# Kernel optimization log

Measured on AMD Instinct MI355X. Metric: run time of the kernel, lower is better.

Reference implementation:

```python
import jax, jax.numpy as jnp
import numpy as np
import math

B, S, D, H = 4, 1024, 1024, 16
DK = D // H


def setup_inputs() -> dict:
    key = jax.random.key(0)
    ks = jax.random.split(key, 14)
    inp = {
        "query": jax.random.normal(ks[0], (B, S, D), dtype=jnp.float32),
        "key": jax.random.normal(ks[1], (B, S, D), dtype=jnp.float32),
        "value": jax.random.normal(ks[2], (B, S, D), dtype=jnp.float32),
        "attention_bias": jax.random.normal(ks[3], (B, S, S, H), dtype=jnp.float32),
        "mask": jax.random.randint(ks[4], (B, S), 0, 2).astype(bool),
    }
    scale = 0.02
    inp["Wq"] = jax.random.normal(ks[5], (D, D), dtype=jnp.float32) * scale
    inp["bq"] = jnp.zeros((D,), dtype=jnp.float32)
    inp["Wk"] = jax.random.normal(ks[6], (D, D), dtype=jnp.float32) * scale
    inp["bk"] = jnp.zeros((D,), dtype=jnp.float32)
    inp["Wv"] = jax.random.normal(ks[7], (D, D), dtype=jnp.float32) * scale
    inp["bv"] = jnp.zeros((D,), dtype=jnp.float32)
    inp["Wo"] = jax.random.normal(ks[8], (D, D), dtype=jnp.float32) * scale
    inp["bo"] = jnp.zeros((D,), dtype=jnp.float32)
    return inp


def reference(query, key, value, attention_bias, mask, Wq, bq, Wk, bk, Wv, bv, Wo, bo):
    # projections (torch Linear: x @ W.T + b), split heads -> [B,H,S,DK]
    def proj(x, W, b):
        y = x @ W.T + b
        return y.reshape(B, S, H, DK).transpose(0, 2, 1, 3)

    q = proj(query, Wq, bq)
    k = proj(key, Wk, bk)
    v = proj(value, Wv, bv)

    bias = attention_bias.transpose(0, 3, 1, 2)  # [B,H,S,S]
    scores = (jnp.einsum("bhqd,bhkd->bhqk", q, k) + bias) / math.sqrt(DK)

    # pairwise mask: outer product of per-token mask, broadcast over heads
    pm = (mask[:, None, :, None] & mask[:, None, None, :])  # [B,1,S,S]
    scores = jnp.where(pm, scores, jnp.float32(-1e9))

    p_attn = jax.nn.softmax(scores, axis=-1)  # dropout is identity in eval
    x = jnp.einsum("bhqk,bhkd->bhqd", p_attn, v)
    x = x.transpose(0, 2, 1, 3).reshape(B, S, D)
    return x @ Wo.T + bo
```

## Files before the change

kernel.cpp:

```cpp
#include <hip/hip_runtime.h>
#include <hip/hip_bf16.h>
#include <math.h>

#define B_ 4
#define S_ 1024
#define D_ 1024
#define H_ 16
#define DK_ 64

typedef short bf16x8 __attribute__((ext_vector_type(8)));
typedef float f32x4 __attribute__((ext_vector_type(4)));

#define MFMA(a, b, c) __builtin_amdgcn_mfma_f32_16x16x32_bf16(a, b, c, 0, 0, 0)

#define GLDS(gp, lp)                                                        \
    __builtin_amdgcn_global_load_lds(                                       \
        (const __attribute__((address_space(1))) void*)(const void*)(gp),   \
        (__attribute__((address_space(3))) void*)(void*)(lp), 16, 0, 0)

static __device__ __forceinline__ unsigned short f2bf(float f) {
    __hip_bfloat16 h = __float2bfloat16(f);
    return *reinterpret_cast<unsigned short*>(&h);
}
static __device__ __forceinline__ float bf2f(unsigned short u) {
    unsigned int x = ((unsigned int)u) << 16;
    union { unsigned int i; float f; } c; c.i = x; return c.f;
}

__global__ __launch_bounds__(256) void cvt3(
    const float* __restrict__ a, const float* __restrict__ b, const float* __restrict__ c,
    unsigned short* __restrict__ oa, unsigned short* __restrict__ ob, unsigned short* __restrict__ oc)
{
    int bx = blockIdx.x;
    int which = bx >> 12;
    const float* in = which == 0 ? a : which == 1 ? b : c;
    unsigned short* out = which == 0 ? oa : which == 1 ? ob : oc;
    int i = (bx & 4095) * 256 + threadIdx.x;
    float4 v = ((const float4*)in)[i];
    ushort4 o;
    o.x = f2bf(v.x); o.y = f2bf(v.y); o.z = f2bf(v.z); o.w = f2bf(v.w);
    ((ushort4*)out)[i] = o;
}

__global__ __launch_bounds__(256) void cvt4(
    const float* __restrict__ a, const float* __restrict__ b,
    const float* __restrict__ c, const float* __restrict__ d,
    unsigned short* __restrict__ oa, unsigned short* __restrict__ ob,
    unsigned short* __restrict__ oc, unsigned short* __restrict__ od)
{
    int bx = blockIdx.x;
    int which = bx >> 10;
    const float* in = which == 0 ? a : which == 1 ? b : which == 2 ? c : d;
    unsigned short* out = which == 0 ? oa : which == 1 ? ob : which == 2 ? oc : od;
    int i = (bx & 1023) * 256 + threadIdx.x;
    float4 v = ((const float4*)in)[i];
    ushort4 o;
    o.x = f2bf(v.x); o.y = f2bf(v.y); o.z = f2bf(v.z); o.w = f2bf(v.w);
    ((ushort4*)out)[i] = o;
}

__global__ __launch_bounds__(256) void prep_bias(
    const float* __restrict__ bias, const int* __restrict__ mask,
    unsigned short* __restrict__ biasP)
{
    const int t = threadIdx.x;
    const int h = t & 15, u = t >> 4;
    const int x = blockIdx.x;
    const int kt = x & 15, q16 = (x >> 4) & 63, b = x >> 10;

    const unsigned short NEG = f2bf(-28672.f);

    int mk[4];
    #pragma unroll
    for (int j = 0; j < 4; ++j) mk[j] = mask[b * 1024 + kt * 64 + j * 16 + u];

    const float* bb = bias + (((size_t)(b * 1024 + q16 * 16) * 1024) + kt * 64) * 16 + h;
    unsigned short* ob = biasP + ((((size_t)(b * 16 + h) * 64 + q16) * 16 + kt) * 64) * 16;

    #pragma unroll
    for (int quad = 0; quad < 4; ++quad) {
        bf16x8 v0, v1;
        #pragma unroll
        for (int r = 0; r < 4; ++r) {
            int q = quad * 4 + r;
            int mq = mask[b * 1024 + q16 * 16 + q];
            #pragma unroll
            for (int j = 0; j < 4; ++j) {
                float v = bb[((size_t)q * 1024 + j * 16 + u) * 16];
                unsigned short pv = (mq && mk[j]) ? f2bf(v * 0.125f) : NEG;
                if (j < 2) v0[j * 4 + r] = (short)pv;
                else       v1[(j - 2) * 4 + r] = (short)pv;
            }
        }
        unsigned short* dst = ob + (size_t)(quad * 16 + u) * 16;
        *(bf16x8*)(dst) = v0;
        *(bf16x8*)(dst + 8) = v1;
    }
}

__global__ __launch_bounds__(256, 2) void gemm128(
    const unsigned short* __restrict__ X0, const unsigned short* __restrict__ X1,
    const unsigned short* __restrict__ X2,
    const unsigned short* __restrict__ W0, const unsigned short* __restrict__ W1,
    const unsigned short* __restrict__ W2,
    const float* __restrict__ bv0, const float* __restrict__ bv1,
    const float* __restrict__ bv2,
    void* __restrict__ Y0, void* __restrict__ Y1, void* __restrict__ Y2,
    const int* __restrict__ mask, int mode_ovr)
{
    __shared__ unsigned short As[128 * 32];
    __shared__ unsigned short Bs[128 * 32];

    const int z = blockIdx.z;
    const unsigned short* X = z == 0 ? X0 : z == 1 ? X1 : X2;
    const unsigned short* W = z == 0 ? W0 : z == 1 ? W1 : W2;
    const float* bvec = z == 0 ? bv0 : z == 1 ? bv1 : bv2;
    void* Yv = z == 0 ? Y0 : z == 1 ? Y1 : Y2;
    const int mode = mode_ovr >= 0 ? mode_ovr : z;

    const int t = threadIdx.x;
    const int w = t >> 6, l = t & 63;
    const int lane16 = l & 15, quad = l >> 4;
    const int m0 = blockIdx.y * 128, n0 = blockIdx.x * 128;
    const int wr = w >> 1, wc = w & 1;

    const int srow = w * 16 + (l >> 2);
    const unsigned short* agp = X + (size_t)(m0 + srow) * 1024 + (l & 3) * 8;
    const unsigned short* bgp = W + (size_t)(n0 + srow) * 1024 + (l & 3) * 8;
    unsigned short* alp = As + w * 512 + l * 8;
    unsigned short* blp = Bs + w * 512 + l * 8;

    f32x4 zero = {0.f, 0.f, 0.f, 0.f};
    f32x4 acc[4][4];
    #pragma unroll
    for (int i = 0; i < 4; ++i)
        #pragma unroll
        for (int j = 0; j < 4; ++j) acc[i][j] = zero;

    for (int kt = 0; kt < 1024; kt += 32) {
        GLDS(agp + kt, alp);
        GLDS(agp + kt + 64 * 1024, alp + 2048);
        GLDS(bgp + kt, blp);
        GLDS(bgp + kt + 64 * 1024, blp + 2048);
        __syncthreads();

        bf16x8 af[4], bfv[4];
        #pragma unroll
        for (int i = 0; i < 4; ++i)
            af[i] = *(const bf16x8*)(As + (wr * 64 + i * 16 + lane16) * 32 + quad * 8);
        #pragma unroll
        for (int j = 0; j < 4; ++j)
            bfv[j] = *(const bf16x8*)(Bs + (wc * 64 + j * 16 + lane16) * 32 + quad * 8);

        #pragma unroll
        for (int i = 0; i < 4; ++i)
            #pragma unroll
            for (int j = 0; j < 4; ++j)
                acc[i][j] = MFMA(af[i], bfv[j], acc[i][j]);
        __syncthreads();
    }

    float bvl[4];
    #pragma unroll
    for (int j = 0; j < 4; ++j) bvl[j] = bvec[n0 + wc * 64 + j * 16 + lane16];

    if (mode == 2) {
        const int bb = m0 >> 10;
        const int sb = (m0 & 1023) + wr * 64;
        #pragma unroll
        for (int i = 0; i < 4; ++i) {
            #pragma unroll
            for (int j = 0; j < 4; ++j) {
                int n = n0 + wc * 64 + j * 16 + lane16;
                ushort4 pk;
                pk.x = f2bf(acc[i][j][0] + bvl[j]);
                pk.y = f2bf(acc[i][j][1] + bvl[j]);
                pk.z = f2bf(acc[i][j][2] + bvl[j]);
                pk.w = f2bf(acc[i][j][3] + bvl[j]);
                int s = sb + i * 16 + quad * 4;
                *(ushort4*)((unsigned short*)Yv + ((size_t)(bb * 1024 + n)) * 1024 + s) = pk;
            }
        }
    } else if (mode == 3) {
        float* Y = (float*)Yv;
        #pragma unroll
        for (int i = 0; i < 4; ++i)
            #pragma unroll
            for (int j = 0; j < 4; ++j) {
                int n = n0 + wc * 64 + j * 16 + lane16;
                #pragma unroll
                for (int r = 0; r < 4; ++r) {
                    size_t m = m0 + wr * 64 + i * 16 + quad * 4 + r;
                    Y[m * 1024 + n] = acc[i][j][r] + bvl[j];
                }
            }
    } else {
        unsigned short* Y = (unsigned short*)Yv;
        #pragma unroll
        for (int i = 0; i < 4; ++i) {
            int mrow[4];
            #pragma unroll
            for (int r = 0; r < 4; ++r)
                mrow[r] = (mode == 0) ? mask[m0 + wr * 64 + i * 16 + quad * 4 + r] : 1;
            #pragma unroll
            for (int j = 0; j < 4; ++j) {
                int n = n0 + wc * 64 + j * 16 + lane16;
                #pragma unroll
                for (int r = 0; r < 4; ++r) {
                    size_t m = m0 + wr * 64 + i * 16 + quad * 4 + r;
                    float val = acc[i][j][r] + bvl[j];
                    if (mode == 0) val = mrow[r] ? val * 0.125f : 0.f;
                    Y[m * 1024 + n] = f2bf(val);
                }
            }
        }
    }
}

__global__ __launch_bounds__(256, 2) void attn_mfma(
    const unsigned short* __restrict__ Qp, const unsigned short* __restrict__ Kp,
    const unsigned short* __restrict__ VpT, const unsigned short* __restrict__ biasP,
    unsigned short* __restrict__ Xp)
{
    __shared__ unsigned short Ks[64 * 64];
    __shared__ unsigned short Vs[64 * 64];
    __shared__ unsigned short Ps[4][16 * 72];

    const int t = threadIdx.x;
    const int w = t >> 6, l = t & 63;
    const int lane16 = l & 15, quad = l >> 4;

    const int bid = blockIdx.x;
    const int bh = bid & 63, qt = bid >> 6;
    const int h = bh & 15, b = bh >> 4;
    const int q0 = qt * 64;
    const int qrow0 = q0 + w * 16;
    const int q16 = qt * 4 + w;

    bf16x8 qf[2];
    #pragma unroll
    for (int c = 0; c < 2; ++c)
        qf[c] = *(const bf16x8*)(Qp + (size_t)(b * 1024 + qrow0 + lane16) * 1024
                                 + h * 64 + c * 32 + quad * 8);

    const unsigned short* bp = biasP
        + ((((size_t)(b * 16 + h) * 64 + q16) * 16) * 64 + l) * 16;

    const int krow = w * 8 + (l >> 3);
    const int kgran = (l & 7) ^ ((l >> 3) & 7);
    const unsigned short* kg = Kp + (size_t)(b * 1024 + krow) * 1024 + h * 64 + kgran * 8;
    unsigned short* klp = Ks + w * 512 + l * 8;
    const unsigned short* vg = VpT + ((size_t)(b * 16 + h) * 64 + krow) * 1024 + kgran * 8;
    unsigned short* vlp = Vs + w * 512 + l * 8;

    f32x4 zero = {0.f, 0.f, 0.f, 0.f};
    f32x4 o[4];
    #pragma unroll
    for (int j = 0; j < 4; ++j) o[j] = zero;
    float m_i[4] = {-1e30f, -1e30f, -1e30f, -1e30f};
    float l_i[4] = {0.f, 0.f, 0.f, 0.f};

    for (int kt16 = 0; kt16 < 16; ++kt16) {
        const int k0 = kt16 * 64;
        GLDS(kg + (size_t)k0 * 1024, klp);
        GLDS(kg + (size_t)(k0 + 32) * 1024, klp + 32 * 64);
        GLDS(vg + k0, vlp);
        GLDS(vg + k0 + 32 * 1024, vlp + 32 * 64);

        bf16x8 bfr0 = *(const bf16x8*)(bp + (size_t)kt16 * 1024);
        bf16x8 bfr1 = *(const bf16x8*)(bp + (size_t)kt16 * 1024 + 8);
        __syncthreads();

        f32x4 s[4];
        #pragma unroll
        for (int j = 0; j < 4; ++j) {
            s[j] = zero;
            #pragma unroll
            for (int c = 0; c < 2; ++c) {
                bf16x8 kf = *(const bf16x8*)(Ks + (j * 16 + lane16) * 64
                                             + (((c * 4 + quad) ^ (lane16 & 7)) * 8));
                s[j] = MFMA(qf[c], kf, s[j]);
            }
        }

        float sc[4][4];
        #pragma unroll
        for (int e = 0; e < 8; ++e) {
            sc[e >> 2][e & 3]       = s[e >> 2][e & 3]       + bf2f((unsigned short)bfr0[e]);
            sc[2 + (e >> 2)][e & 3] = s[2 + (e >> 2)][e & 3] + bf2f((unsigned short)bfr1[e]);
        }

        float p[4][4];
        #pragma unroll
        for (int r = 0; r < 4; ++r) {
            float mx = fmaxf(fmaxf(sc[0][r], sc[1][r]), fmaxf(sc[2][r], sc[3][r]));
            #pragma unroll
            for (int d = 1; d < 16; d <<= 1) mx = fmaxf(mx, __shfl_xor(mx, d, 64));
            float mnew = fmaxf(m_i[r], mx);
            float alpha = __expf(m_i[r] - mnew);
            m_i[r] = mnew;
            float sum = 0.f;
            #pragma unroll
            for (int j = 0; j < 4; ++j) {
                p[j][r] = __expf(sc[j][r] - mnew);
                sum += p[j][r];
            }
            #pragma unroll
            for (int d = 1; d < 16; d <<= 1) sum += __shfl_xor(sum, d, 64);
            l_i[r] = l_i[r] * alpha + sum;
            #pragma unroll
            for (int jd = 0; jd < 4; ++jd) o[jd][r] *= alpha;
        }

        #pragma unroll
        for (int j = 0; j < 4; ++j)
            #pragma unroll
            for (int r = 0; r < 4; ++r)
                Ps[w][(quad * 4 + r) * 72 + j * 16 + lane16] = f2bf(p[j][r]);
        asm volatile("" ::: "memory");

        bf16x8 pf[2];
        #pragma unroll
        for (int c = 0; c < 2; ++c)
            pf[c] = *(const bf16x8*)(&Ps[w][lane16 * 72 + c * 32 + quad * 8]);

        #pragma unroll
        for (int jd = 0; jd < 4; ++jd)
            #pragma unroll
            for (int c = 0; c < 2; ++c) {
                bf16x8 vf = *(const bf16x8*)(Vs + (jd * 16 + lane16) * 64
                                             + (((c * 4 + quad) ^ (lane16 & 7)) * 8));
                o[jd] = MFMA(pf[c], vf, o[jd]);
            }
        __syncthreads();
    }

    float inv[4];
    #pragma unroll
    for (int r = 0; r < 4; ++r) inv[r] = 1.0f / l_i[r];

    #pragma unroll
    for (int jd = 0; jd < 4; ++jd)
        #pragma unroll
        for (int r = 0; r < 4; ++r)
            Xp[(size_t)(b * 1024 + qrow0 + quad * 4 + r) * 1024
               + h * 64 + jd * 16 + lane16] = f2bf(o[jd][r] * inv[r]);
}

extern "C" void kernel_launch(void* const* d_in, const int* in_sizes, int n_in,
                              void* d_out, int out_size, void* d_ws, size_t ws_size,
                              hipStream_t stream)
{
    const float* query = (const float*)d_in[0];
    const float* key   = (const float*)d_in[1];
    const float* value = (const float*)d_in[2];
    const float* abias = (const float*)d_in[3];
    const int*   mask  = (const int*)d_in[4];
    const float* Wq = (const float*)d_in[5];
    const float* bq = (const float*)d_in[6];
    const float* Wk = (const float*)d_in[7];
    const float* bk = (const float*)d_in[8];
    const float* Wv = (const float*)d_in[9];
    const float* bv = (const float*)d_in[10];
    const float* Wo = (const float*)d_in[11];
    const float* bo = (const float*)d_in[12];
    float* out = (float*)d_out;

    const size_t T = (size_t)B_ * S_ * D_;
    const size_t WSZ = (size_t)D_ * D_;
    const size_t BPSZ = (size_t)B_ * H_ * S_ * S_;
    unsigned short* p = (unsigned short*)d_ws;
    unsigned short* biasP = p;  p += BPSZ;
    unsigned short* qb  = p;  p += T;
    unsigned short* kb  = p;  p += T;
    unsigned short* vb  = p;  p += T;
    unsigned short* wqb = p;  p += WSZ;
    unsigned short* wkb = p;  p += WSZ;
    unsigned short* wvb = p;  p += WSZ;
    unsigned short* wob = p;  p += WSZ;
    unsigned short* Qpj = p;  p += T;
    unsigned short* Kpj = p;  p += T;
    unsigned short* VpT = p;  p += T;
    unsigned short* Xpj = p;  p += T;

    cvt3<<<dim3(3 * 4096), 256, 0, stream>>>(query, key, value, qb, kb, vb);
    cvt4<<<dim3(4 * 1024), 256, 0, stream>>>(Wq, Wk, Wv, Wo, wqb, wkb, wvb, wob);
    prep_bias<<<dim3(4096), 256, 0, stream>>>(abias, mask, biasP);

    gemm128<<<dim3(8, 32, 3), 256, 0, stream>>>(
        qb, kb, vb, wqb, wkb, wvb, bq, bk, bv,
        (void*)Qpj, (void*)Kpj, (void*)VpT, mask, -1);

    attn_mfma<<<dim3(1024), 256, 0, stream>>>(Qpj, Kpj, VpT, biasP, Xpj);

    gemm128<<<dim3(8, 32, 1), 256, 0, stream>>>(
        Xpj, Xpj, Xpj, wob, wob, wob, bo, bo, bo,
        (void*)out, (void*)out, (void*)out, mask, 3);
}
```

Baseline: 583.5 us.

## Merge prep kernels, interleave bias prep with QKV GEMM, double-buffer attention K/V

Merges the two conversion kernels into one launch. Interleaves the memory-bound bias/mask preprocessing blocks with the compute-bound QKV projection blocks in a single grid so the two can overlap. The attention kernel now double-buffers K/V tiles in LDS, prefetches the next bias fragment, drops the trailing barrier and uses an XOR swizzle for the P scratch buffer. The output projection switches to 128x64 tiles to double the block count. This trades more LDS and register pressure, plus a heterogeneous block mix, for better overlap and occupancy.

```diff
diff --git a/kernel.cpp b/kernel.cpp
--- a/kernel.cpp
+++ b/kernel.cpp
@@ -27,192 +27,177 @@
     union { unsigned int i; float f; } c; c.i = x; return c.f;
 }
 
-__global__ __launch_bounds__(256) void cvt3(
+__global__ __launch_bounds__(256) void cvt_all(
     const float* __restrict__ a, const float* __restrict__ b, const float* __restrict__ c,
-    unsigned short* __restrict__ oa, unsigned short* __restrict__ ob, unsigned short* __restrict__ oc)
+    const float* __restrict__ wa, const float* __restrict__ wb,
+    const float* __restrict__ wc, const float* __restrict__ wd,
+    unsigned short* __restrict__ oa, unsigned short* __restrict__ ob, unsigned short* __restrict__ oc,
+    unsigned short* __restrict__ owa, unsigned short* __restrict__ owb,
+    unsigned short* __restrict__ owc, unsigned short* __restrict__ owd)
 {
     int bx = blockIdx.x;
-    int which = bx >> 12;
-    const float* in = which == 0 ? a : which == 1 ? b : c;
-    unsigned short* out = which == 0 ? oa : which == 1 ? ob : oc;
-    int i = (bx & 4095) * 256 + threadIdx.x;
+    const float* in; unsigned short* out; int i;
+    if (bx < 12288) {
+        int which = bx >> 12;
+        in  = which == 0 ? a : which == 1 ? b : c;
+        out = which == 0 ? oa : which == 1 ? ob : oc;
+        i = (bx & 4095) * 256 + threadIdx.x;
+    } else {
+        int b2 = bx - 12288;
+        int which = b2 >> 10;
+        in  = which == 0 ? wa : which == 1 ? wb : which == 2 ? wc : wd;
+        out = which == 0 ? owa : which == 1 ? owb : which == 2 ? owc : owd;
+        i = (b2 & 1023) * 256 + threadIdx.x;
+    }
     float4 v = ((const float4*)in)[i];
     ushort4 o;
     o.x = f2bf(v.x); o.y = f2bf(v.y); o.z = f2bf(v.z); o.w = f2bf(v.w);
     ((ushort4*)out)[i] = o;
 }
 
-__global__ __launch_bounds__(256) void cvt4(
-    const float* __restrict__ a, const float* __restrict__ b,
-    const float* __restrict__ c, const float* __restrict__ d,
-    unsigned short* __restrict__ oa, unsigned short* __restrict__ ob,
-    unsigned short* __restrict__ oc, unsigned short* __restrict__ od)
-{
-    int bx = blockIdx.x;
-    int which = bx >> 10;
-    const float* in = which == 0 ? a : which == 1 ? b : which == 2 ? c : d;
-    unsigned short* out = which == 0 ? oa : which == 1 ? ob : which == 2 ? oc : od;
-    int i = (bx & 1023) * 256 + threadIdx.x;
-    float4 v = ((const float4*)in)[i];
-    ushort4 o;
-    o.x = f2bf(v.x); o.y = f2bf(v.y); o.z = f2bf(v.z); o.w = f2bf(v.w);
-    ((ushort4*)out)[i] = o;
-}
-
-__global__ __launch_bounds__(256) void prep_bias(
-    const float* __restrict__ bias, const int* __restrict__ mask,
-    unsigned short* __restrict__ biasP)
-{
-    const int t = threadIdx.x;
-    const int h = t & 15, u = t >> 4;
-    const int x = blockIdx.x;
-    const int kt = x & 15, q16 = (x >> 4) & 63, b = x >> 10;
-
-    const unsigned short NEG = f2bf(-28672.f);
-
-    int mk[4];
-    #pragma unroll
-    for (int j = 0; j < 4; ++j) mk[j] = mask[b * 1024 + kt * 64 + j * 16 + u];
-
-    const float* bb = bias + (((size_t)(b * 1024 + q16 * 16) * 1024) + kt * 64) * 16 + h;
-    unsigned short* ob = biasP + ((((size_t)(b * 16 + h) * 64 + q16) * 16 + kt) * 64) * 16;
-
-    #pragma unroll
-    for (int quad = 0; quad < 4; ++quad) {
-        bf16x8 v0, v1;
-        #pragma unroll
-        for (int r = 0; r < 4; ++r) {
-            int q = quad * 4 + r;
-            int mq = mask[b * 1024 + q16 * 16 + q];
-            #pragma unroll
-            for (int j = 0; j < 4; ++j) {
-                float v = bb[((size_t)q * 1024 + j * 16 + u) * 16];
-                unsigned short pv = (mq && mk[j]) ? f2bf(v * 0.125f) : NEG;
-                if (j < 2) v0[j * 4 + r] = (short)pv;
-                else       v1[(j - 2) * 4 + r] = (short)pv;
-            }
-        }
-        unsigned short* dst = ob + (size_t)(quad * 16 + u) * 16;
-        *(bf16x8*)(dst) = v0;
-        *(bf16x8*)(dst + 8) = v1;
-    }
-}
-
-__global__ __launch_bounds__(256, 2) void gemm128(
+__global__ __launch_bounds__(256, 2) void qkv_prep(
     const unsigned short* __restrict__ X0, const unsigned short* __restrict__ X1,
     const unsigned short* __restrict__ X2,
     const unsigned short* __restrict__ W0, const unsigned short* __restrict__ W1,
     const unsigned short* __restrict__ W2,
     const float* __restrict__ bv0, const float* __restrict__ bv1,
     const float* __restrict__ bv2,
-    void* __restrict__ Y0, void* __restrict__ Y1, void* __restrict__ Y2,
-    const int* __restrict__ mask, int mode_ovr)
+    unsigned short* __restrict__ Y0, unsigned short* __restrict__ Y1,
+    unsigned short* __restrict__ Y2,
+    const float* __restrict__ bias, const int* __restrict__ mask,
+    unsigned short* __restrict__ biasP)
 {
     __shared__ unsigned short As[128 * 32];
     __shared__ unsigned short Bs[128 * 32];
 
-    const int z = blockIdx.z;
-    const unsigned short* X = z == 0 ? X0 : z == 1 ? X1 : X2;
-    const unsigned short* W = z == 0 ? W0 : z == 1 ? W1 : W2;
-    const float* bvec = z == 0 ? bv0 : z == 1 ? bv1 : bv2;
-    void* Yv = z == 0 ? Y0 : z == 1 ? Y1 : Y2;
-    const int mode = mode_ovr >= 0 ? mode_ovr : z;
-
     const int t = threadIdx.x;
-    const int w = t >> 6, l = t & 63;
-    const int lane16 = l & 15, quad = l >> 4;
-    const int m0 = blockIdx.y * 128, n0 = blockIdx.x * 128;
-    const int wr = w >> 1, wc = w & 1;
-
-    const int srow = w * 16 + (l >> 2);
-    const unsigned short* agp = X + (size_t)(m0 + srow) * 1024 + (l & 3) * 8;
-    const unsigned short* bgp = W + (size_t)(n0 + srow) * 1024 + (l & 3) * 8;
-    unsigned short* alp = As + w * 512 + l * 8;
-    unsigned short* blp = Bs + w * 512 + l * 8;
-
-    f32x4 zero = {0.f, 0.f, 0.f, 0.f};
-    f32x4 acc[4][4];
-    #pragma unroll
-    for (int i = 0; i < 4; ++i)
-        #pragma unroll
-        for (int j = 0; j < 4; ++j) acc[i][j] = zero;
-
-    for (int kt = 0; kt < 1024; kt += 32) {
-        GLDS(agp + kt, alp);
-        GLDS(agp + kt + 64 * 1024, alp + 2048);
-        GLDS(bgp + kt, blp);
-        GLDS(bgp + kt + 64 * 1024, blp + 2048);
-        __syncthreads();
-
-        bf16x8 af[4], bfv[4];
+    const int bid = blockIdx.x;
+    const int grp = bid / 19, rr = bid - grp * 19;
+
+    if (rr < 3) {
+        const int gi = grp * 3 + rr;
+        const int z = gi >> 8;
+        const int rem = gi & 255;
+        const int n0 = (rem & 7) * 128, m0 = (rem >> 3) * 128;
+
+        const unsigned short* X = z == 0 ? X0 : z == 1 ? X1 : X2;
+        const unsigned short* W = z == 0 ? W0 : z == 1 ? W1 : W2;
+        const float* bvec = z == 0 ? bv0 : z == 1 ? bv1 : bv2;
+        unsigned short* Y = z == 0 ? Y0 : z == 1 ? Y1 : Y2;
+
+        const int w = t >> 6, l = t & 63;
+        const int lane16 = l & 15, quad = l >> 4;
+        const int wr = w >> 1, wc = w & 1;
+
+        const int srow = w * 16 + (l >> 2);
+        const unsigned short* agp = X + (size_t)(m0 + srow) * 1024 + (l & 3) * 8;
+        const unsigned short* bgp = W + (size_t)(n0 + srow) * 1024 + (l & 3) * 8;
+        unsigned short* alp = As + w * 512 + l * 8;
+        unsigned short* blp = Bs + w * 512 + l * 8;
+
+        f32x4 zero = {0.f, 0.f, 0.f, 0.f};
+        f32x4 acc[4][4];
         #pragma unroll
         for (int i = 0; i < 4; ++i)
-            af[i] = *(const bf16x8*)(As + (wr * 64 + i * 16 + lane16) * 32 + quad * 8);
-        #pragma unroll
-        for (int j = 0; j < 4; ++j)
-            bfv[j] = *(const bf16x8*)(Bs + (wc * 64 + j * 16 + lane16) * 32 + quad * 8);
-
-        #pragma unroll
-        for (int i = 0; i < 4; ++i)
+            #pragma unroll
+            for (int j = 0; j < 4; ++j) acc[i][j] = zero;
+
+        for (int kt = 0; kt < 1024; kt += 32) {
+            GLDS(agp + kt, alp);
+            GLDS(agp + kt + 64 * 1024, alp + 2048);
+            GLDS(bgp + kt, blp);
+            GLDS(bgp + kt + 64 * 1024, blp + 2048);
+            __syncthreads();
+
+            bf16x8 af[4], bfv[4];
+            #pragma unroll
+            for (int i = 0; i < 4; ++i)
+                af[i] = *(const bf16x8*)(As + (wr * 64 + i * 16 + lane16) * 32 + quad * 8);
             #pragma unroll
             for (int j = 0; j < 4; ++j)
-                acc[i][j] = MFMA(af[i], bfv[j], acc[i][j]);
-        __syncthreads();
-    }
-
-    float bvl[4];
-    #pragma unroll
-    for (int j = 0; j < 4; ++j) bvl[j] = bvec[n0 + wc * 64 + j * 16 + lane16];
-
-    if (mode == 2) {
-        const int bb = m0 >> 10;
-        const int sb = (m0 & 1023) + wr * 64;
-        #pragma unroll
-        for (int i = 0; i < 4; ++i) {
-            #pragma unroll
-            for (int j = 0; j < 4; ++j) {
-                int n = n0 + wc * 64 + j * 16 + lane16;
-                ushort4 pk;
-                pk.x = f2bf(acc[i][j][0] + bvl[j]);
-                pk.y = f2bf(acc[i][j][1] + bvl[j]);
-                pk.z = f2bf(acc[i][j][2] + bvl[j]);
-                pk.w = f2bf(acc[i][j][3] + bvl[j]);
-                int s = sb + i * 16 + quad * 4;
-                *(ushort4*)((unsigned short*)Yv + ((size_t)(bb * 1024 + n)) * 1024 + s) = pk;
-            }
-        }
-    } else if (mode == 3) {
-        float* Y = (float*)Yv;
-        #pragma unroll
-        for (int i = 0; i < 4; ++i)
-            #pragma unroll
-            for (int j = 0; j < 4; ++j) {
-                int n = n0 + wc * 64 + j * 16 + lane16;
+                bfv[j] = *(const bf16x8*)(Bs + (wc * 64 + j * 16 + lane16) * 32 + quad * 8);
+
+            #pragma unroll
+            for (int i = 0; i < 4; ++i)
                 #pragma unroll
-                for (int r = 0; r < 4; ++r) {
-                    size_t m = m0 + wr * 64 + i * 16 + quad * 4 + r;
-                    Y[m * 1024 + n] = acc[i][j][r] + bvl[j];
+                for (int j = 0; j < 4; ++j)
+                    acc[i][j] = MFMA(af[i], bfv[j], acc[i][j]);
+            __syncthreads();
+        }
+
+        float bvl[4];
+        #pragma unroll
+        for (int j = 0; j < 4; ++j) bvl[j] = bvec[n0 + wc * 64 + j * 16 + lane16];
+
+        if (z == 2) {
+            const int bb = m0 >> 10;
+            const int sb = (m0 & 1023) + wr * 64;
+            #pragma unroll
+            for (int i = 0; i < 4; ++i) {
+                #pragma unroll
+                for (int j = 0; j < 4; ++j) {
+                    int n = n0 + wc * 64 + j * 16 + lane16;
+                    ushort4 pk;
+                    pk.x = f2bf(acc[i][j][0] + bvl[j]);
+                    pk.y = f2bf(acc[i][j][1] + bvl[j]);
+                    pk.z = f2bf(acc[i][j][2] + bvl[j]);
+                    pk.w = f2bf(acc[i][j][3] + bvl[j]);
+                    int s = sb + i * 16 + quad * 4;
+                    *(ushort4*)(Y + ((size_t)(bb * 1024 + n)) * 1024 + s) = pk;
                 }
             }
+        } else {
+            #pragma unroll
+            for (int i = 0; i < 4; ++i) {
+                int mrow[4];
+                #pragma unroll
+                for (int r = 0; r < 4; ++r)
+                    mrow[r] = (z == 0) ? mask[m0 + wr * 64 + i * 16 + quad * 4 + r] : 1;
+                #pragma unroll
+                for (int j = 0; j < 4; ++j) {
+                    int n = n0 + wc * 64 + j * 16 + lane16;
+                    #pragma unroll
+                    for (int r = 0; r < 4; ++r) {
+                        size_t m = m0 + wr * 64 + i * 16 + quad * 4 + r;
+                        float val = acc[i][j][r] + bvl[j];
+                        if (z == 0) val = mrow[r] ? val * 0.125f : 0.f;
+                        Y[m * 1024 + n] = f2bf(val);
+                    }
+                }
+            }
+        }
     } else {
-        unsigned short* Y = (unsigned short*)Yv;
-        #pragma unroll
-        for (int i = 0; i < 4; ++i) {
-            int mrow[4];
-            #pragma unroll
-            for (int r = 0; r < 4; ++r)
-                mrow[r] = (mode == 0) ? mask[m0 + wr * 64 + i * 16 + quad * 4 + r] : 1;
-            #pragma unroll
-            for (int j = 0; j < 4; ++j) {
-                int n = n0 + wc * 64 + j * 16 + lane16;
+        const int pidx = grp * 16 + (rr - 3);
+        const int hh = t & 15, u = t >> 4;
+        const int kt = pidx & 15, q16 = (pidx >> 4) & 63, bb = pidx >> 10;
+
+        const unsigned short NEG = f2bf(-28672.f);
+
+        int mk[4];
+        #pragma unroll
+        for (int j = 0; j < 4; ++j) mk[j] = mask[bb * 1024 + kt * 64 + j * 16 + u];
+
+        const float* bbp = bias + (((size_t)(bb * 1024 + q16 * 16) * 1024) + kt * 64) * 16 + hh;
+        unsigned short* obp = biasP + ((((size_t)(bb * 16 + hh) * 64 + q16) * 16 + kt) * 64) * 16;
+
+        #pragma unroll
+        for (int quad = 0; quad < 4; ++quad) {
+            bf16x8 v0, v1;
+            #pragma unroll
+            for (int r = 0; r < 4; ++r) {
+                int q = quad * 4 + r;
+                int mq = mask[bb * 1024 + q16 * 16 + q];
                 #pragma unroll
-                for (int r = 0; r < 4; ++r) {
-                    size_t m = m0 + wr * 64 + i * 16 + quad * 4 + r;
-                    float val = acc[i][j][r] + bvl[j];
-                    if (mode == 0) val = mrow[r] ? val * 0.125f : 0.f;
-                    Y[m * 1024 + n] = f2bf(val);
+                for (int j = 0; j < 4; ++j) {
+                    float v = bbp[((size_t)q * 1024 + j * 16 + u) * 16];
+                    unsigned short pv = (mq && mk[j]) ? f2bf(v * 0.125f) : NEG;
+                    if (j < 2) v0[j * 4 + r] = (short)pv;
+                    else       v1[(j - 2) * 4 + r] = (short)pv;
                 }
             }
+            unsigned short* dst = obp + (size_t)(quad * 16 + u) * 16;
+            *(bf16x8*)(dst) = v0;
+            *(bf16x8*)(dst + 8) = v1;
         }
     }
 }
@@ -222,9 +207,9 @@
     const unsigned short* __restrict__ VpT, const unsigned short* __restrict__ biasP,
     unsigned short* __restrict__ Xp)
 {
-    __shared__ unsigned short Ks[64 * 64];
-    __shared__ unsigned short Vs[64 * 64];
-    __shared__ unsigned short Ps[4][16 * 72];
+    __shared__ unsigned short Ks[2][64 * 64];
+    __shared__ unsigned short Vs[2][64 * 64];
+    __shared__ unsigned short Ps[4][16 * 64];
 
     const int t = threadIdx.x;
     const int w = t >> 6, l = t & 63;
@@ -249,9 +234,16 @@
     const int krow = w * 8 + (l >> 3);
     const int kgran = (l & 7) ^ ((l >> 3) & 7);
     const unsigned short* kg = Kp + (size_t)(b * 1024 + krow) * 1024 + h * 64 + kgran * 8;
-    unsigned short* klp = Ks + w * 512 + l * 8;
     const unsigned short* vg = VpT + ((size_t)(b * 16 + h) * 64 + krow) * 1024 + kgran * 8;
-    unsigned short* vlp = Vs + w * 512 + l * 8;
+    unsigned short* kst = &Ks[0][w * 512 + l * 8];
+    unsigned short* vst = &Vs[0][w * 512 + l * 8];
+
+    GLDS(kg, kst);
+    GLDS(kg + (size_t)32 * 1024, kst + 32 * 64);
+    GLDS(vg, vst);
+    GLDS(vg + (size_t)32 * 1024, vst + 32 * 64);
+    bf16x8 bfr0 = *(const bf16x8*)(bp);
+    bf16x8 bfr1 = *(const bf16x8*)(bp + 8);
 
     f32x4 zero = {0.f, 0.f, 0.f, 0.f};
     f32x4 o[4];
@@ -260,16 +252,24 @@
     float m_i[4] = {-1e30f, -1e30f, -1e30f, -1e30f};
     float l_i[4] = {0.f, 0.f, 0.f, 0.f};
 
+    char* psb = (char*)&Ps[w][0];
+
     for (int kt16 = 0; kt16 < 16; ++kt16) {
-        const int k0 = kt16 * 64;
-        GLDS(kg + (size_t)k0 * 1024, klp);
-        GLDS(kg + (size_t)(k0 + 32) * 1024, klp + 32 * 64);
-        GLDS(vg + k0, vlp);
-        GLDS(vg + k0 + 32 * 1024, vlp + 32 * 64);
-
-        bf16x8 bfr0 = *(const bf16x8*)(bp + (size_t)kt16 * 1024);
-        bf16x8 bfr1 = *(const bf16x8*)(bp + (size_t)kt16 * 1024 + 8);
+        const int cur = kt16 & 1;
         __syncthreads();
+
+        if (kt16 < 15) {
+            const size_t kn = (size_t)(kt16 + 1) * 64;
+            unsigned short* kd = kst + (cur ^ 1) * 4096;
+            unsigned short* vd = vst + (cur ^ 1) * 4096;
+            GLDS(kg + kn * 1024, kd);
+            GLDS(kg + (kn + 32) * 1024, kd + 32 * 64);
+            GLDS(vg + kn, vd);
+            GLDS(vg + kn + (size_t)32 * 1024, vd + 32 * 64);
+        }
+
+        const unsigned short* Kc = &Ks[0][0] + cur * 4096;
+        const unsigned short* Vc = &Vs[0][0] + cur * 4096;
 
         f32x4 s[4];
         #pragma unroll
@@ -277,23 +277,27 @@
             s[j] = zero;
             #pragma unroll
             for (int c = 0; c < 2; ++c) {
-                bf16x8 kf = *(const bf16x8*)(Ks + (j * 16 + lane16) * 64
+                bf16x8 kf = *(const bf16x8*)(Kc + (j * 16 + lane16) * 64
                                              + (((c * 4 + quad) ^ (lane16 & 7)) * 8));
                 s[j] = MFMA(qf[c], kf, s[j]);
             }
         }
 
-        float sc[4][4];
         #pragma unroll
         for (int e = 0; e < 8; ++e) {
-            sc[e >> 2][e & 3]       = s[e >> 2][e & 3]       + bf2f((unsigned short)bfr0[e]);
-            sc[2 + (e >> 2)][e & 3] = s[2 + (e >> 2)][e & 3] + bf2f((unsigned short)bfr1[e]);
+            s[e >> 2][e & 3]       += bf2f((unsigned short)bfr0[e]);
+            s[2 + (e >> 2)][e & 3] += bf2f((unsigned short)bfr1[e]);
+        }
+
+        if (kt16 < 15) {
+            bfr0 = *(const bf16x8*)(bp + (size_t)(kt16 + 1) * 1024);
+            bfr1 = *(const bf16x8*)(bp + (size_t)(kt16 + 1) * 1024 + 8);
         }
 
         float p[4][4];
         #pragma unroll
         for (int r = 0; r < 4; ++r) {
-            float mx = fmaxf(fmaxf(sc[0][r], sc[1][r]), fmaxf(sc[2][r], sc[3][r]));
+            float mx = fmaxf(fmaxf(s[0][r], s[1][r]), fmaxf(s[2][r], s[3][r]));
             #pragma unroll
             for (int d = 1; d < 16; d <<= 1) mx = fmaxf(mx, __shfl_xor(mx, d, 64));
             float mnew = fmaxf(m_i[r], mx);
@@ -302,7 +306,7 @@
             float sum = 0.f;
             #pragma unroll
             for (int j = 0; j < 4; ++j) {
-                p[j][r] = __expf(sc[j][r] - mnew);
+                p[j][r] = __expf(s[j][r] - mnew);
                 sum += p[j][r];
             }
             #pragma unroll
@@ -315,24 +319,28 @@
         #pragma unroll
         for (int j = 0; j < 4; ++j)
             #pragma unroll
-            for (int r = 0; r < 4; ++r)
-                Ps[w][(quad * 4 + r) * 72 + j * 16 + lane16] = f2bf(p[j][r]);
+            for (int r = 0; r < 4; ++r) {
+                int row = quad * 4 + r;
+                int cb = (j * 16 + lane16) * 2;
+                *(unsigned short*)(psb + row * 128 + (cb ^ ((row & 7) << 4))) = f2bf(p[j][r]);
+            }
         asm volatile("" ::: "memory");
 
         bf16x8 pf[2];
         #pragma unroll
-        for (int c = 0; c < 2; ++c)
-            pf[c] = *(const bf16x8*)(&Ps[w][lane16 * 72 + c * 32 + quad * 8]);
+        for (int c = 0; c < 2; ++c) {
+            int cb = c * 64 + quad * 16;
+            pf[c] = *(const bf16x8*)(psb + lane16 * 128 + (cb ^ ((lane16 & 7) << 4)));
+        }
 
         #pragma unroll
         for (int jd = 0; jd < 4; ++jd)
             #pragma unroll
             for (int c = 0; c < 2; ++c) {
-                bf16x8 vf = *(const bf16x8*)(Vs + (jd * 16 + lane16) * 64
+                bf16x8 vf = *(const bf16x8*)(Vc + (jd * 16 + lane16) * 64
                                              + (((c * 4 + quad) ^ (lane16 & 7)) * 8));
                 o[jd] = MFMA(pf[c], vf, o[jd]);
             }
-        __syncthreads();
     }
 
     float inv[4];
@@ -345,6 +353,71 @@
         for (int r = 0; r < 4; ++r)
             Xp[(size_t)(b * 1024 + qrow0 + quad * 4 + r) * 1024
                + h * 64 + jd * 16 + lane16] = f2bf(o[jd][r] * inv[r]);
+}
+
+__global__ __launch_bounds__(256, 2) void gemm_o64(
+    const unsigned short* __restrict__ X, const unsigned short* __restrict__ W,
+    const float* __restrict__ bvec, float* __restrict__ Y)
+{
+    __shared__ unsigned short As[128 * 32];
+    __shared__ unsigned short Bs[64 * 32];
+
+    const int t = threadIdx.x;
+    const int w = t >> 6, l = t & 63;
+    const int lane16 = l & 15, quad = l >> 4;
+    const int m0 = blockIdx.y * 128, n0 = blockIdx.x * 64;
+    const int wr = w >> 1, wc = w & 1;
+
+    const int srow = w * 16 + (l >> 2);
+    const unsigned short* agp = X + (size_t)(m0 + srow) * 1024 + (l & 3) * 8;
+    const unsigned short* bgp = W + (size_t)(n0 + srow) * 1024 + (l & 3) * 8;
+    unsigned short* alp = As + w * 512 + l * 8;
+    unsigned short* blp = Bs + w * 512 + l * 8;
+
+    f32x4 zero = {0.f, 0.f, 0.f, 0.f};
+    f32x4 acc[4][2];
+    #pragma unroll
+    for (int i = 0; i < 4; ++i)
+        #pragma unroll
+        for (int j = 0; j < 2; ++j) acc[i][j] = zero;
+
+    for (int kt = 0; kt < 1024; kt += 32) {
+        GLDS(agp + kt, alp);
+        GLDS(agp + kt + 64 * 1024, alp + 2048);
+        GLDS(bgp + kt, blp);
+        __syncthreads();
+
+        bf16x8 af[4], bfv[2];
+        #pragma unroll
+        for (int i = 0; i < 4; ++i)
+            af[i] = *(const bf16x8*)(As + (wr * 64 + i * 16 + lane16) * 32 + quad * 8);
+        #pragma unroll
+        for (int j = 0; j < 2; ++j)
+            bfv[j] = *(const bf16x8*)(Bs + (wc * 32 + j * 16 + lane16) * 32 + quad * 8);
+
+        #pragma unroll
+        for (int i = 0; i < 4; ++i)
+            #pragma unroll
+            for (int j = 0; j < 2; ++j)
+                acc[i][j] = MFMA(af[i], bfv[j], acc[i][j]);
+        __syncthreads();
+    }
+
+    float bvl[2];
+    #pragma unroll
+    for (int j = 0; j < 2; ++j) bvl[j] = bvec[n0 + wc * 32 + j * 16 + lane16];
+
+    #pragma unroll
+    for (int i = 0; i < 4; ++i)
+        #pragma unroll
+        for (int j = 0; j < 2; ++j) {
+            int n = n0 + wc * 32 + j * 16 + lane16;
+            #pragma unroll
+            for (int r = 0; r < 4; ++r) {
+                size_t m = m0 + wr * 64 + i * 16 + quad * 4 + r;
+                Y[m * 1024 + n] = acc[i][j][r] + bvl[j];
+            }
+        }
 }
 
 extern "C" void kernel_launch(void* const* d_in, const int* in_sizes, int n_in,
@@ -383,17 +456,15 @@
     unsigned short* VpT = p;  p += T;
     unsigned short* Xpj = p;  p += T;
 
-    cvt3<<<dim3(3 * 4096), 256, 0, stream>>>(query, key, value, qb, kb, vb);
-    cvt4<<<dim3(4 * 1024), 256, 0, stream>>>(Wq, Wk, Wv, Wo, wqb, wkb, wvb, wob);
-    prep_bias<<<dim3(4096), 256, 0, stream>>>(abias, mask, biasP);
-
-    gemm128<<<dim3(8, 32, 3), 256, 0, stream>>>(
+    cvt_all<<<dim3(16384), 256, 0, stream>>>(
+        query, key, value, Wq, Wk, Wv, Wo,
+        qb, kb, vb, wqb, wkb, wvb, wob);
+
+    qkv_prep<<<dim3(4864), 256, 0, stream>>>(
         qb, kb, vb, wqb, wkb, wvb, bq, bk, bv,
-        (void*)Qpj, (void*)Kpj, (void*)VpT, mask, -1);
+        Qpj, Kpj, VpT, abias, mask, biasP);
 
     attn_mfma<<<dim3(1024), 256, 0, stream>>>(Qpj, Kpj, VpT, biasP, Xpj);
 
-    gemm128<<<dim3(8, 32, 1), 256, 0, stream>>>(
-        Xpj, Xpj, Xpj, wob, wob, wob, bo, bo, bo,
-        (void*)out, (void*)out, (void*)out, mask, 3);
-}
+    gemm_o64<<<dim3(16, 32), 256, 0, stream>>>(Xpj, wob, bo, out);
+}
```

New measurement: 601.7 us. +3.1%, slower.
